# Performance work log

Hardware: AMD Instinct MI355X
Metric: run time of the kernel (lower is better)

## Reference

```python
import jax, jax.numpy as jnp
import numpy as np

B, H, S, D = 1, 16, 4096, 64


def setup_inputs() -> dict:
    key = jax.random.key(0)
    kq, kk, kv = jax.random.split(key, 3)
    Q = jax.random.normal(kq, (B, H, S, D), dtype=jnp.float32)
    K = jax.random.normal(kk, (B, H, S, D), dtype=jnp.float32)
    V = jax.random.normal(kv, (B, H, S, D), dtype=jnp.float32)
    # causal mask, broadcast over batch/heads: True = attend
    mask = jnp.tril(jnp.ones((S, S), dtype=bool))[None, None, :, :]
    return {"Q": Q, "K": K, "V": V, "mask": mask}


def reference(Q, K, V, mask):
    d_k = Q.shape[-1]
    scale = 1.0 / jnp.sqrt(jnp.asarray(d_k, dtype=Q.dtype))
    # [..., q, k] scores; mask==False positions set to -inf before softmax
    scores = jnp.einsum('...qd,...kd->...qk', Q, K) * scale
    scores = jnp.where(mask, scores, jnp.asarray(-jnp.inf, dtype=scores.dtype))
    attn = jax.nn.softmax(scores, axis=-1)
    return jnp.einsum('...qk,...kd->...qd', attn, V)
```

## Files before the change

### kernel.cpp

```cpp
#include <hip/hip_runtime.h>
#include <hip/hip_bf16.h>

typedef __attribute__((ext_vector_type(8))) short short8;
typedef __attribute__((ext_vector_type(4))) short s4v;
typedef __attribute__((ext_vector_type(4))) int   int4v;
typedef __attribute__((ext_vector_type(4))) float floatx4;

#define MFMA16(A,B,C) __builtin_amdgcn_mfma_f32_16x16x32_bf16(A,B,C,0,0,0)

__device__ __forceinline__ short bf16bits(float x) {
    __hip_bfloat16 h = __float2bfloat16(x);
    return *(short*)&h;
}
__device__ __forceinline__ short8 cvt8(const float* p) {
    floatx4 a = *(const floatx4*)p;
    floatx4 b = *(const floatx4*)(p + 4);
    short8 r;
    r[0]=bf16bits(a.x); r[1]=bf16bits(a.y); r[2]=bf16bits(a.z); r[3]=bf16bits(a.w);
    r[4]=bf16bits(b.x); r[5]=bf16bits(b.y); r[6]=bf16bits(b.z); r[7]=bf16bits(b.w);
    return r;
}
__device__ __forceinline__ short8 cvt8s(const float* p) {
    constexpr float SCL2 = 0.125f * 1.44269504088896f;
    floatx4 a = *(const floatx4*)p;
    floatx4 b = *(const floatx4*)(p + 4);
    a *= SCL2; b *= SCL2;
    short8 r;
    r[0]=bf16bits(a.x); r[1]=bf16bits(a.y); r[2]=bf16bits(a.z); r[3]=bf16bits(a.w);
    r[4]=bf16bits(b.x); r[5]=bf16bits(b.y); r[6]=bf16bits(b.z); r[7]=bf16bits(b.w);
    return r;
}
__device__ __forceinline__ int pk2(float lo, float hi) {
    int r;
    asm("v_cvt_pk_bf16_f32 %0, %1, %2" : "=v"(r) : "v"(lo), "v"(hi));
    return r;
}

__global__ __launch_bounds__(256) void prep(const float* __restrict__ V,
                                            short* __restrict__ VT,
                                            const float* __restrict__ K,
                                            short* __restrict__ K16, int doK)
{
    __shared__ short tile[64 * 65];
    const int t  = threadIdx.x;
    const int h  = blockIdx.x >> 6;
    const int s0 = (blockIdx.x & 63) << 6;
    const float* src = V + ((size_t)h * 4096 + s0) * 64;
    const int r = t >> 4, dq = (t & 15) * 4;
#pragma unroll
    for (int pass = 0; pass < 4; ++pass) {
        const int s = pass * 16 + r;
        floatx4 f = *(const floatx4*)(src + s * 64 + dq);
        short* w = tile + s * 65 + dq;
        w[0] = bf16bits(f.x); w[1] = bf16bits(f.y);
        w[2] = bf16bits(f.z); w[3] = bf16bits(f.w);
    }
    __syncthreads();
    const int d = t >> 2, sc = (t & 3) * 16;
    short8 a, b;
#pragma unroll
    for (int j = 0; j < 8; ++j) a[j] = tile[(sc + j) * 65 + d];
#pragma unroll
    for (int j = 0; j < 8; ++j) b[j] = tile[(sc + 8 + j) * 65 + d];
    short* dst = VT + ((size_t)h * 64 + d) * 4096 + s0 + sc;
    *(short8*)dst       = a;
    *(short8*)(dst + 8) = b;
    if (doK) {
        const size_t base = (size_t)blockIdx.x * 4096 + (size_t)t * 16;
        *(short8*)(K16 + base)     = cvt8(K + base);
        *(short8*)(K16 + base + 8) = cvt8(K + base + 8);
    }
}

template<bool KB16>
__global__ __attribute__((amdgpu_waves_per_eu(4, 4))) __launch_bounds__(256)
void attn_fast(const float* __restrict__ Qg, const float* __restrict__ Kg,
               const short* __restrict__ K16g, const short* __restrict__ VTg,
               float* __restrict__ Og)
{
    constexpr int S = 4096, D = 64;

    __shared__ __align__(16) short lK[8192];
    __shared__ __align__(16) short lV[8192];

    const int tid = threadIdx.x;
    const int wv  = tid >> 6;
    const int ln  = tid & 63;
    const int ll  = ln & 15;
    const int qd  = ln >> 4;
    const int qhalf = wv & 1;
    const int khalf = wv >> 1;

    const int c = blockIdx.x & 255;
    const int s = blockIdx.x >> 8;
    const int h = c & 15;
    const int x = c >> 4;
    const int qblk = (s == 0) ? (63 - x) : (s == 1) ? (32 + x) : (s == 2) ? (31 - x) : x;
    const int qb   = qblk << 6;
    const int qrow = qb + (qhalf << 5);

    const float* Qh  = Qg  + (size_t)h * S * D;
    const float* Kf  = Kg  + (size_t)h * S * D;
    const short* K16 = K16g + (size_t)h * S * D;
    const short* Vt  = VTg + (size_t)h * 64 * S;

    short8 qA0, qA1, qB0, qB1;
    {
        const float* qp = Qh + (qrow + ll) * D + qd * 8;
        qA0 = cvt8s(qp);       qA1 = cvt8s(qp + 32);
        const float* qp2 = qp + 16 * D;
        qB0 = cvt8s(qp2);      qB1 = cvt8s(qp2 + 32);
    }

    floatx4 oA[4], oB[4], olA, olB;
#pragma unroll
    for (int dt = 0; dt < 4; ++dt) { oA[dt] = (floatx4){0.f,0.f,0.f,0.f}; oB[dt] = oA[dt]; }
    olA = (floatx4){0.f,0.f,0.f,0.f};
    olB = olA;

    short8 ones;
#pragma unroll
    for (int j = 0; j < 8; ++j) ones[j] = (short)0x3F80;

    const int kkey = tid >> 3, kd8 = tid & 7;
    const int koct = kd8 & 3;
    short* kdst = lK + ((kkey >> 4) * 2 + (kd8 >> 2)) * 512
                     + ((((kkey & 15) | (koct << 4)) ^ (koct * 5)) * 8);
    const float* ksrcf = Kf  + kkey * 64 + kd8 * 8;
    const short* ksrc6 = K16 + kkey * 64 + kd8 * 8;
    const int vd = tid >> 2, voct = tid & 3;
    short* vdst = lV + (vd >> 4) * 512
                     + ((((vd & 15) | (voct << 4)) ^ (voct * 5)) * 8);
    const short* vsrc = Vt + (size_t)vd * S + voct * 8;
    const int rblk = ((ll | (qd << 4)) ^ (qd * 5));

    const int kv_end = qb + 64;
    const int wv_end = qrow + 32;

    auto ldK = [&](int kv) -> short8 {
        return KB16 ? *(const short8*)(ksrc6 + kv * 64) : cvt8(ksrcf + kv * 64);
    };

    auto mkpf = [&](floatx4 sc0, floatx4 sc1, int qgrp, int kvh) -> short8 {
        float p0[4], p1[4];
#pragma unroll
        for (int r = 0; r < 4; ++r) { p0[r] = exp2f(sc0[r]); p1[r] = exp2f(sc1[r]); }
        if (kvh + 31 > qgrp) {
            const int qg = qgrp + ll;
            const int k0 = kvh + qd * 4, k1 = k0 + 16;
#pragma unroll
            for (int r = 0; r < 4; ++r) {
                if (k0 + r > qg) p0[r] = 0.f;
                if (k1 + r > qg) p1[r] = 0.f;
            }
        }
        int w0 = pk2(p0[0], p0[1]);
        int w1 = pk2(p0[2], p0[3]);
        int w2 = pk2(p1[0], p1[1]);
        int w3 = pk2(p1[2], p1[3]);
        asm("v_permlane32_swap_b32 %0, %1" : "+v"(w0), "+v"(w2));
        asm("v_permlane32_swap_b32 %0, %1" : "+v"(w1), "+v"(w3));
        asm("v_permlane16_swap_b32 %0, %1" : "+v"(w0), "+v"(w2));
        asm("v_permlane16_swap_b32 %0, %1" : "+v"(w1), "+v"(w3));
        int4v pv = {w0, w1, w2, w3};
        return *(short8*)&pv;
    };

    short8 kp0 = ldK(0),  kp1 = ldK(32);
    short8 vp0 = *(const short8*)(vsrc);
    short8 vp1 = *(const short8*)(vsrc + 32);

    const int ntiles = kv_end >> 6;
    int bo = 0;
    for (int t = 0; t <= ntiles; ++t) {
        __syncthreads();
        if (t < ntiles) {
            *(short8*)(kdst + bo)        = kp0;
            *(short8*)(kdst + bo + 2048) = kp1;
            *(short8*)(vdst + bo)        = vp0;
            *(short8*)(vdst + bo + 2048) = vp1;
            const int nk = (t + 1) << 6;
            if (nk < kv_end) {
                kp0 = ldK(nk);
                kp1 = ldK(nk + 32);
                vp0 = *(const short8*)(vsrc + nk);
                vp1 = *(const short8*)(vsrc + nk + 32);
            }
        }
        if (t > 0) {
            const int kv  = (t - 1) << 6;
            const int kvw = kv + (khalf << 5);
            if (kvw < wv_end) {
                const int ro = (bo ^ 4096) + (khalf << 11);
                const short* Kb = lK + ro;
                const short* Vb = lV + ro;
                floatx4 zz = (floatx4){0.f,0.f,0.f,0.f};
                floatx4 sA0=zz, sA1=zz, sB0=zz, sB1=zz;
                short8 kf;
                __builtin_amdgcn_s_setprio(1);
                kf = ((const short8*)(Kb +    0))[rblk]; sA0 = MFMA16(kf, qA0, sA0); sB0 = MFMA16(kf, qB0, sB0);
                kf = ((const short8*)(Kb +  512))[rblk]; sA0 = MFMA16(kf, qA1, sA0); sB0 = MFMA16(kf, qB1, sB0);
                kf = ((const short8*)(Kb + 1024))[rblk]; sA1 = MFMA16(kf, qA0, sA1); sB1 = MFMA16(kf, qB0, sB1);
                kf = ((const short8*)(Kb + 1536))[rblk]; sA1 = MFMA16(kf, qA1, sA1); sB1 = MFMA16(kf, qB1, sB1);
                __builtin_amdgcn_s_setprio(0);

                short8 pfA = mkpf(sA0, sA1, qrow,      kvw);
                short8 pfB = mkpf(sB0, sB1, qrow + 16, kvw);
                __builtin_amdgcn_s_setprio(1);
#pragma unroll
                for (int dt = 0; dt < 4; ++dt) {
                    short8 vf = ((const short8*)(Vb + dt * 512))[rblk];
                    oA[dt] = MFMA16(pfA, vf, oA[dt]);
                    oB[dt] = MFMA16(pfB, vf, oB[dt]);
                }
                olA = MFMA16(pfA, ones, olA);
                olB = MFMA16(pfB, ones, olB);
                __builtin_amdgcn_s_setprio(0);
            }
        }
        bo ^= 4096;
    }

    __syncthreads();
    float* sAod = (float*)lK;
    float* sBod = (float*)lV;
    const int mbase = ((qhalf << 6) + ln) * 20;
    if (khalf == 1) {
#pragma unroll
        for (int dt = 0; dt < 4; ++dt)
#pragma unroll
            for (int r = 0; r < 4; ++r) {
                sAod[mbase + dt * 4 + r] = oA[dt][r];
                sBod[mbase + dt * 4 + r] = oB[dt][r];
            }
#pragma unroll
        for (int r = 0; r < 4; ++r) {
            sAod[mbase + 16 + r] = olA[r];
            sBod[mbase + 16 + r] = olB[r];
        }
    }
    __syncthreads();
    if (khalf == 0) {
#pragma unroll
        for (int dt = 0; dt < 4; ++dt)
#pragma unroll
            for (int r = 0; r < 4; ++r) {
                oA[dt][r] += sAod[mbase + dt * 4 + r];
                oB[dt][r] += sBod[mbase + dt * 4 + r];
            }
#pragma unroll
        for (int r = 0; r < 4; ++r) {
            olA[r] += sAod[mbase + 16 + r];
            olB[r] += sBod[mbase + 16 + r];
        }
#pragma unroll
        for (int r = 0; r < 4; ++r) {
            const float rl = 1.f / fmaxf(olA[r], 1e-37f);
            const int q = qrow + qd * 4 + r;
            float* op = Og + ((size_t)h * S + q) * D + ll;
#pragma unroll
            for (int dt = 0; dt < 4; ++dt)
                op[dt * 16] = oA[dt][r] * rl;
        }
#pragma unroll
        for (int r = 0; r < 4; ++r) {
            const float rl = 1.f / fmaxf(olB[r], 1e-37f);
            const int q = qrow + 16 + qd * 4 + r;
            float* op = Og + ((size_t)h * S + q) * D + ll;
#pragma unroll
            for (int dt = 0; dt < 4; ++dt)
                op[dt * 16] = oB[dt][r] * rl;
        }
    }
}

__global__ __launch_bounds__(256, 4)
void attn_legacy(const float* __restrict__ Qg, const float* __restrict__ Kg,
                 const float* __restrict__ Vg, float* __restrict__ Og)
{
    constexpr int S = 4096, D = 64;
    constexpr float SCL2 = 0.125f * 1.44269504088896f;
    constexpr float NEG  = -1.0e30f;
    __shared__ __align__(16) short lK[2048];
    __shared__ __align__(16) short lV[2048];
    __shared__ __align__(16) short lP[2048];
    const int tid = threadIdx.x, wv = tid >> 6, ln = tid & 63, ll = ln & 15, qd = ln >> 4;
    const int bid = blockIdx.x, h = bid & 15, qblk = 63 - (bid >> 4), qb = qblk << 6;
    const float* Qh = Qg + (size_t)h * S * D;
    const float* Kh = Kg + (size_t)h * S * D;
    const float* Vh = Vg + (size_t)h * S * D;
    const int qrow = qb + wv * 16;
    short8 qf0, qf1;
    { const float* qp = Qh + (qrow + ll) * D + qd * 8; qf0 = cvt8(qp); qf1 = cvt8(qp + 32); }
    floatx4 o[4]; float mi[4], li[4];
#pragma unroll
    for (int dt = 0; dt < 4; ++dt) o[dt] = (floatx4){0.f,0.f,0.f,0.f};
#pragma unroll
    for (int r = 0; r < 4; ++r) { mi[r] = NEG; li[r] = 0.f; }
    const int k_st = tid >> 3, dbase = (tid & 7) * 8;
    const int sq = (dbase >> 3) & 3, sks = dbase >> 5;
    const int kw_slot = (((k_st >> 4) * 2 + sks) * 64)
                      + (((sq << 4) | (k_st & 15)) ^ (sq | (sks << 2)));
    const int kr0 = ln ^ qd, kr1 = ln ^ (qd | 4), vbit3 = (ln >> 3) & 1;
    const int kv_end = qb + 64, wv_end = qrow + 16;
    for (int kv = 0; kv < kv_end; kv += 32) {
        __syncthreads();
        {
            short8 kval = cvt8(Kh + (kv + k_st) * D + dbase);
            ((short8*)lK)[kw_slot] = kval;
            short8 vval = cvt8(Vh + (kv + k_st) * D + dbase);
            const int vq = (k_st >> 3) << 4, vj = k_st & 7;
#pragma unroll
            for (int i = 0; i < 8; ++i) {
                int d = dbase + i, dt = d >> 4, l2 = d & 15;
                int lp = (vq | l2) ^ (((l2 >> 3) & 1) | (dt << 1));
                lV[dt * 512 + lp * 8 + vj] = vval[i];
            }
        }
        __syncthreads();
        if (kv < wv_end) {
            floatx4 sc0 = (floatx4){0.f,0.f,0.f,0.f}, sc1 = sc0; short8 kf;
            kf = ((const short8*)lK)[0*64+kr0]; sc0 = MFMA16(qf0, kf, sc0);
            kf = ((const short8*)lK)[1*64+kr1]; sc0 = MFMA16(qf1, kf, sc0);
            kf = ((const short8*)lK)[2*64+kr0]; sc1 = MFMA16(qf0, kf, sc1);
            kf = ((const short8*)lK)[3*64+kr1]; sc1 = MFMA16(qf1, kf, sc1);
            float p0[4], p1[4]; const int qg = qrow + qd * 4;
#pragma unroll
            for (int r = 0; r < 4; ++r) { p0[r] = sc0[r]*SCL2; p1[r] = sc1[r]*SCL2; }
            if (kv + 31 > qrow) {
                const int k0 = kv + ll, k1 = kv + 16 + ll;
#pragma unroll
                for (int r = 0; r < 4; ++r) {
                    if (k0 > qg + r) p0[r] = NEG;
                    if (k1 > qg + r) p1[r] = NEG;
                }
            }
#pragma unroll
            for (int r = 0; r < 4; ++r) {
                float mx = fmaxf(p0[r], p1[r]);
                mx = fmaxf(mx, __shfl_xor(mx,1)); mx = fmaxf(mx, __shfl_xor(mx,2));
                mx = fmaxf(mx, __shfl_xor(mx,4)); mx = fmaxf(mx, __shfl_xor(mx,8));
                const float nm = fmaxf(mi[r], mx);
                const float a = exp2f(mi[r] - nm); mi[r] = nm;
                p0[r] = exp2f(p0[r] - nm); p1[r] = exp2f(p1[r] - nm);
                float ps = p0[r] + p1[r];
                ps += __shfl_xor(ps,1); ps += __shfl_xor(ps,2);
                ps += __shfl_xor(ps,4); ps += __shfl_xor(ps,8);
                li[r] = li[r] * a + ps;
#pragma unroll
                for (int dt = 0; dt < 4; ++dt) o[dt][r] *= a;
            }
            {
                const int pbase = wv * 512 + (ll & 7);
                const int dl0 = ((ll >> 3) << 4) + qd * 4;
#pragma unroll
                for (int r = 0; r < 4; ++r) {
                    lP[pbase + (dl0 + r) * 8]      = bf16bits(p0[r]);
                    lP[pbase + (dl0 + 32 + r) * 8] = bf16bits(p1[r]);
                }
            }
            __threadfence_block();
            short8 pf = ((const short8*)lP)[wv * 64 + ln];
#pragma unroll
            for (int dt = 0; dt < 4; ++dt) {
                short8 vf = ((const short8*)lV)[dt * 64 + (ln ^ (vbit3 | (dt << 1)))];
                o[dt] = MFMA16(pf, vf, o[dt]);
            }
        }
    }
#pragma unroll
    for (int r = 0; r < 4; ++r) {
        const float rl = 1.f / fmaxf(li[r], 1e-30f);
        const int q = qrow + qd * 4 + r;
        float* op = Og + ((size_t)h * S + q) * D + ll;
#pragma unroll
        for (int dt = 0; dt < 4; ++dt) op[dt * 16] = o[dt][r] * rl;
    }
}

extern "C" void kernel_launch(void* const* d_in, const int* in_sizes, int n_in,
                              void* d_out, int out_size, void* d_ws, size_t ws_size,
                              hipStream_t stream) {
    const float* Q = (const float*)d_in[0];
    const float* K = (const float*)d_in[1];
    const float* V = (const float*)d_in[2];
    float* O = (float*)d_out;
    const size_t elems  = (size_t)16 * 4096 * 64;
    const size_t oneBuf = elems * sizeof(short);
    if (ws_size >= 2 * oneBuf) {
        short* VT  = (short*)d_ws;
        short* K16 = (short*)d_ws + elems;
        prep<<<dim3(1024), dim3(256), 0, stream>>>(V, VT, K, K16, 1);
        attn_fast<true><<<dim3(1024), dim3(256), 0, stream>>>(Q, K, K16, VT, O);
    } else if (ws_size >= oneBuf) {
        short* VT = (short*)d_ws;
        prep<<<dim3(1024), dim3(256), 0, stream>>>(V, VT, K, VT, 0);
        attn_fast<false><<<dim3(1024), dim3(256), 0, stream>>>(Q, K, nullptr, VT, O);
    } else {
        attn_legacy<<<dim3(1024), dim3(256), 0, stream>>>(Q, K, V, O);
    }
}
```

Measured before the change: 184.4 us.

## Split long causal query blocks across two KV halves and merge partials

Adds an attn_split kernel in which the heaviest causal query blocks (indices 33–63) are each processed by two workgroups. Each workgroup covers half of the key/value range and writes unnormalized partial outputs and row sums to workspace. A merge_split kernel then adds the partials and normalizes them. This targets the tail imbalance where the longest query blocks set the kernel time, at the cost of an extra launch, more blocks and extra global traffic for the partials. It is only used when the workspace is large enough for the partial buffers.

```diff
diff --git a/kernel.cpp b/kernel.cpp
--- a/kernel.cpp
+++ b/kernel.cpp
@@ -72,6 +72,258 @@
     }
 }
 
+__global__ __attribute__((amdgpu_waves_per_eu(4, 4))) __launch_bounds__(256)
+void attn_split(const float* __restrict__ Qg, const short* __restrict__ K16g,
+                const short* __restrict__ VTg, float* __restrict__ Og,
+                float* __restrict__ partO, float* __restrict__ partL)
+{
+    constexpr int S = 4096, D = 64;
+
+    __shared__ __align__(16) short lK[8192];
+    __shared__ __align__(16) short lV[8192];
+
+    const int tid = threadIdx.x;
+    const int wv  = tid >> 6;
+    const int ln  = tid & 63;
+    const int ll  = ln & 15;
+    const int qd  = ln >> 4;
+    const int qhalf = wv & 1;
+    const int khalf = wv >> 1;
+
+    const int bid = blockIdx.x;
+    const int h = bid / 95;
+    const int u = bid % 95;
+    int qblk, ks, ke, slot;
+    if (u < 62) {
+        qblk = 63 - (u >> 1);
+        const int part = u & 1;
+        const int T = qblk + 1, Th = T >> 1;
+        ks = part ? Th : 0;
+        ke = part ? T : Th;
+        slot = (h * 31 + (qblk - 33)) * 2 + part;
+    } else {
+        qblk = 94 - u;
+        ks = 0; ke = qblk + 1;
+        slot = -1;
+    }
+    const int qb   = qblk << 6;
+    const int qrow = qb + (qhalf << 5);
+
+    const float* Qh  = Qg  + (size_t)h * S * D;
+    const short* K16 = K16g + (size_t)h * S * D;
+    const short* Vt  = VTg + (size_t)h * 64 * S;
+
+    short8 qA0, qA1, qB0, qB1;
+    {
+        const float* qp = Qh + (qrow + ll) * D + qd * 8;
+        qA0 = cvt8s(qp);       qA1 = cvt8s(qp + 32);
+        const float* qp2 = qp + 16 * D;
+        qB0 = cvt8s(qp2);      qB1 = cvt8s(qp2 + 32);
+    }
+
+    floatx4 oA[4], oB[4], olA, olB;
+#pragma unroll
+    for (int dt = 0; dt < 4; ++dt) { oA[dt] = (floatx4){0.f,0.f,0.f,0.f}; oB[dt] = oA[dt]; }
+    olA = (floatx4){0.f,0.f,0.f,0.f};
+    olB = olA;
+
+    short8 ones;
+#pragma unroll
+    for (int j = 0; j < 8; ++j) ones[j] = (short)0x3F80;
+
+    const int kkey = tid >> 3, kd8 = tid & 7;
+    const int koct = kd8 & 3;
+    short* kdst = lK + ((kkey >> 4) * 2 + (kd8 >> 2)) * 512
+                     + ((((kkey & 15) | (koct << 4)) ^ (koct * 5)) * 8);
+    const short* ksrc6 = K16 + kkey * 64 + kd8 * 8;
+    const int vd = tid >> 2, voct = tid & 3;
+    short* vdst = lV + (vd >> 4) * 512
+                     + ((((vd & 15) | (voct << 4)) ^ (voct * 5)) * 8);
+    const short* vsrc = Vt + (size_t)vd * S + voct * 8;
+    const int rblk = ((ll | (qd << 4)) ^ (qd * 5));
+
+    const int wv_end = qrow + 32;
+
+    auto mkpf = [&](floatx4 sc0, floatx4 sc1, int qgrp, int kvh) -> short8 {
+        float p0[4], p1[4];
+#pragma unroll
+        for (int r = 0; r < 4; ++r) { p0[r] = exp2f(sc0[r]); p1[r] = exp2f(sc1[r]); }
+        if (kvh + 31 > qgrp) {
+            const int qg = qgrp + ll;
+            const int k0 = kvh + qd * 4, k1 = k0 + 16;
+#pragma unroll
+            for (int r = 0; r < 4; ++r) {
+                if (k0 + r > qg) p0[r] = 0.f;
+                if (k1 + r > qg) p1[r] = 0.f;
+            }
+        }
+        int w0 = pk2(p0[0], p0[1]);
+        int w1 = pk2(p0[2], p0[3]);
+        int w2 = pk2(p1[0], p1[1]);
+        int w3 = pk2(p1[2], p1[3]);
+        asm("v_permlane32_swap_b32 %0, %1" : "+v"(w0), "+v"(w2));
+        asm("v_permlane32_swap_b32 %0, %1" : "+v"(w1), "+v"(w3));
+        asm("v_permlane16_swap_b32 %0, %1" : "+v"(w0), "+v"(w2));
+        asm("v_permlane16_swap_b32 %0, %1" : "+v"(w1), "+v"(w3));
+        int4v pv = {w0, w1, w2, w3};
+        return *(short8*)&pv;
+    };
+
+    short8 kp0 = *(const short8*)(ksrc6 + ks * 64 * 64);
+    short8 kp1 = *(const short8*)(ksrc6 + (ks * 64 + 32) * 64);
+    short8 vp0 = *(const short8*)(vsrc + ks * 64);
+    short8 vp1 = *(const short8*)(vsrc + ks * 64 + 32);
+
+    int bo = 0;
+    for (int t = ks; t <= ke; ++t) {
+        __syncthreads();
+        if (t < ke) {
+            *(short8*)(kdst + bo)        = kp0;
+            *(short8*)(kdst + bo + 2048) = kp1;
+            *(short8*)(vdst + bo)        = vp0;
+            *(short8*)(vdst + bo + 2048) = vp1;
+            if (t + 1 < ke) {
+                const int nk = (t + 1) << 6;
+                kp0 = *(const short8*)(ksrc6 + (size_t)nk * 64);
+                kp1 = *(const short8*)(ksrc6 + (size_t)(nk + 32) * 64);
+                vp0 = *(const short8*)(vsrc + nk);
+                vp1 = *(const short8*)(vsrc + nk + 32);
+            }
+        }
+        if (t > ks) {
+            const int kv  = (t - 1) << 6;
+            const int kvw = kv + (khalf << 5);
+            if (kvw < wv_end) {
+                const int ro = (bo ^ 4096) + (khalf << 11);
+                const short* Kb = lK + ro;
+                const short* Vb = lV + ro;
+                floatx4 zz = (floatx4){0.f,0.f,0.f,0.f};
+                floatx4 sA0=zz, sA1=zz, sB0=zz, sB1=zz;
+                short8 kf;
+                __builtin_amdgcn_s_setprio(1);
+                kf = ((const short8*)(Kb +    0))[rblk]; sA0 = MFMA16(kf, qA0, sA0); sB0 = MFMA16(kf, qB0, sB0);
+                kf = ((const short8*)(Kb +  512))[rblk]; sA0 = MFMA16(kf, qA1, sA0); sB0 = MFMA16(kf, qB1, sB0);
+                kf = ((const short8*)(Kb + 1024))[rblk]; sA1 = MFMA16(kf, qA0, sA1); sB1 = MFMA16(kf, qB0, sB1);
+                kf = ((const short8*)(Kb + 1536))[rblk]; sA1 = MFMA16(kf, qA1, sA1); sB1 = MFMA16(kf, qB1, sB1);
+                __builtin_amdgcn_s_setprio(0);
+
+                short8 pfA = mkpf(sA0, sA1, qrow,      kvw);
+                short8 pfB = mkpf(sB0, sB1, qrow + 16, kvw);
+                __builtin_amdgcn_s_setprio(1);
+#pragma unroll
+                for (int dt = 0; dt < 4; ++dt) {
+                    short8 vf = ((const short8*)(Vb + dt * 512))[rblk];
+                    oA[dt] = MFMA16(pfA, vf, oA[dt]);
+                    oB[dt] = MFMA16(pfB, vf, oB[dt]);
+                }
+                olA = MFMA16(pfA, ones, olA);
+                olB = MFMA16(pfB, ones, olB);
+                __builtin_amdgcn_s_setprio(0);
+            }
+        }
+        bo ^= 4096;
+    }
+
+    __syncthreads();
+    float* sAod = (float*)lK;
+    float* sBod = (float*)lV;
+    const int mbase = ((qhalf << 6) + ln) * 20;
+    if (khalf == 1) {
+#pragma unroll
+        for (int dt = 0; dt < 4; ++dt)
+#pragma unroll
+            for (int r = 0; r < 4; ++r) {
+                sAod[mbase + dt * 4 + r] = oA[dt][r];
+                sBod[mbase + dt * 4 + r] = oB[dt][r];
+            }
+#pragma unroll
+        for (int r = 0; r < 4; ++r) {
+            sAod[mbase + 16 + r] = olA[r];
+            sBod[mbase + 16 + r] = olB[r];
+        }
+    }
+    __syncthreads();
+    if (khalf == 0) {
+#pragma unroll
+        for (int dt = 0; dt < 4; ++dt)
+#pragma unroll
+            for (int r = 0; r < 4; ++r) {
+                oA[dt][r] += sAod[mbase + dt * 4 + r];
+                oB[dt][r] += sBod[mbase + dt * 4 + r];
+            }
+#pragma unroll
+        for (int r = 0; r < 4; ++r) {
+            olA[r] += sAod[mbase + 16 + r];
+            olB[r] += sBod[mbase + 16 + r];
+        }
+        if (slot < 0) {
+#pragma unroll
+            for (int r = 0; r < 4; ++r) {
+                const float rl = 1.f / fmaxf(olA[r], 1e-37f);
+                const int q = qrow + qd * 4 + r;
+                float* op = Og + ((size_t)h * S + q) * D + ll;
+#pragma unroll
+                for (int dt = 0; dt < 4; ++dt)
+                    op[dt * 16] = oA[dt][r] * rl;
+            }
+#pragma unroll
+            for (int r = 0; r < 4; ++r) {
+                const float rl = 1.f / fmaxf(olB[r], 1e-37f);
+                const int q = qrow + 16 + qd * 4 + r;
+                float* op = Og + ((size_t)h * S + q) * D + ll;
+#pragma unroll
+                for (int dt = 0; dt < 4; ++dt)
+                    op[dt * 16] = oB[dt][r] * rl;
+            }
+        } else {
+            float* po = partO + (size_t)slot * 4096;
+            float* pl = partL + (size_t)slot * 64;
+#pragma unroll
+            for (int r = 0; r < 4; ++r) {
+                const int row = (qhalf << 5) + qd * 4 + r;
+                float* op = po + row * 64 + ll;
+#pragma unroll
+                for (int dt = 0; dt < 4; ++dt)
+                    op[dt * 16] = oA[dt][r];
+                if (ll == 0) pl[row] = olA[r];
+            }
+#pragma unroll
+            for (int r = 0; r < 4; ++r) {
+                const int row = (qhalf << 5) + 16 + qd * 4 + r;
+                float* op = po + row * 64 + ll;
+#pragma unroll
+                for (int dt = 0; dt < 4; ++dt)
+                    op[dt * 16] = oB[dt][r];
+                if (ll == 0) pl[row] = olB[r];
+            }
+        }
+    }
+}
+
+__global__ __launch_bounds__(256) void merge_split(const float* __restrict__ pO,
+                                                   const float* __restrict__ pL,
+                                                   float* __restrict__ Og)
+{
+    const int bid = blockIdx.x;
+    const int h  = bid / 31;
+    const int qb = (33 + bid % 31) << 6;
+    const size_t b0 = (size_t)(bid * 2) * 4096;
+    const int t = threadIdx.x;
+#pragma unroll
+    for (int k = 0; k < 4; ++k) {
+        const int idx = t * 4 + k * 1024;
+        const int row = idx >> 6;
+        floatx4 a = *(const floatx4*)(pO + b0 + idx);
+        floatx4 b = *(const floatx4*)(pO + b0 + 4096 + idx);
+        const float l = pL[bid * 128 + row] + pL[bid * 128 + 64 + row];
+        const float rl = 1.f / fmaxf(l, 1e-37f);
+        floatx4 o;
+        o.x = (a.x + b.x) * rl; o.y = (a.y + b.y) * rl;
+        o.z = (a.z + b.z) * rl; o.w = (a.w + b.w) * rl;
+        *(floatx4*)(Og + ((size_t)h * 4096 + qb + row) * 64 + (idx & 63)) = o;
+    }
+}
+
 template<bool KB16>
 __global__ __attribute__((amdgpu_waves_per_eu(4, 4))) __launch_bounds__(256)
 void attn_fast(const float* __restrict__ Qg, const float* __restrict__ Kg,
@@ -79,10 +331,8 @@
                float* __restrict__ Og)
 {
     constexpr int S = 4096, D = 64;
-
     __shared__ __align__(16) short lK[8192];
     __shared__ __align__(16) short lV[8192];
-
     const int tid = threadIdx.x;
     const int wv  = tid >> 6;
     const int ln  = tid & 63;
@@ -90,7 +340,6 @@
     const int qd  = ln >> 4;
     const int qhalf = wv & 1;
     const int khalf = wv >> 1;
-
     const int c = blockIdx.x & 255;
     const int s = blockIdx.x >> 8;
     const int h = c & 15;
@@ -98,12 +347,10 @@
     const int qblk = (s == 0) ? (63 - x) : (s == 1) ? (32 + x) : (s == 2) ? (31 - x) : x;
     const int qb   = qblk << 6;
     const int qrow = qb + (qhalf << 5);
-
     const float* Qh  = Qg  + (size_t)h * S * D;
     const float* Kf  = Kg  + (size_t)h * S * D;
     const short* K16 = K16g + (size_t)h * S * D;
     const short* Vt  = VTg + (size_t)h * 64 * S;
-
     short8 qA0, qA1, qB0, qB1;
     {
         const float* qp = Qh + (qrow + ll) * D + qd * 8;
@@ -111,17 +358,14 @@
         const float* qp2 = qp + 16 * D;
         qB0 = cvt8s(qp2);      qB1 = cvt8s(qp2 + 32);
     }
-
     floatx4 oA[4], oB[4], olA, olB;
 #pragma unroll
     for (int dt = 0; dt < 4; ++dt) { oA[dt] = (floatx4){0.f,0.f,0.f,0.f}; oB[dt] = oA[dt]; }
     olA = (floatx4){0.f,0.f,0.f,0.f};
     olB = olA;
-
     short8 ones;
 #pragma unroll
     for (int j = 0; j < 8; ++j) ones[j] = (short)0x3F80;
-
     const int kkey = tid >> 3, kd8 = tid & 7;
     const int koct = kd8 & 3;
     short* kdst = lK + ((kkey >> 4) * 2 + (kd8 >> 2)) * 512
@@ -133,14 +377,11 @@
                      + ((((vd & 15) | (voct << 4)) ^ (voct * 5)) * 8);
     const short* vsrc = Vt + (size_t)vd * S + voct * 8;
     const int rblk = ((ll | (qd << 4)) ^ (qd * 5));
-
     const int kv_end = qb + 64;
     const int wv_end = qrow + 32;
-
     auto ldK = [&](int kv) -> short8 {
         return KB16 ? *(const short8*)(ksrc6 + kv * 64) : cvt8(ksrcf + kv * 64);
     };
-
     auto mkpf = [&](floatx4 sc0, floatx4 sc1, int qgrp, int kvh) -> short8 {
         float p0[4], p1[4];
 #pragma unroll
@@ -165,11 +406,9 @@
         int4v pv = {w0, w1, w2, w3};
         return *(short8*)&pv;
     };
-
     short8 kp0 = ldK(0),  kp1 = ldK(32);
     short8 vp0 = *(const short8*)(vsrc);
     short8 vp1 = *(const short8*)(vsrc + 32);
-
     const int ntiles = kv_end >> 6;
     int bo = 0;
     for (int t = 0; t <= ntiles; ++t) {
@@ -203,7 +442,6 @@
                 kf = ((const short8*)(Kb + 1024))[rblk]; sA1 = MFMA16(kf, qA0, sA1); sB1 = MFMA16(kf, qB0, sB1);
                 kf = ((const short8*)(Kb + 1536))[rblk]; sA1 = MFMA16(kf, qA1, sA1); sB1 = MFMA16(kf, qB1, sB1);
                 __builtin_amdgcn_s_setprio(0);
-
                 short8 pfA = mkpf(sA0, sA1, qrow,      kvw);
                 short8 pfB = mkpf(sB0, sB1, qrow + 16, kvw);
                 __builtin_amdgcn_s_setprio(1);
@@ -220,7 +458,6 @@
         }
         bo ^= 4096;
     }
-
     __syncthreads();
     float* sAod = (float*)lK;
     float* sBod = (float*)lV;
@@ -387,7 +624,17 @@
     float* O = (float*)d_out;
     const size_t elems  = (size_t)16 * 4096 * 64;
     const size_t oneBuf = elems * sizeof(short);
-    if (ws_size >= 2 * oneBuf) {
+    const size_t partOB = (size_t)992 * 4096 * sizeof(float);
+    const size_t partLB = (size_t)992 * 64 * sizeof(float);
+    if (ws_size >= 2 * oneBuf + partOB + partLB) {
+        short* VT  = (short*)d_ws;
+        short* K16 = (short*)d_ws + elems;
+        float* pO  = (float*)((char*)d_ws + 2 * oneBuf);
+        float* pL  = pO + (size_t)992 * 4096;
+        prep<<<dim3(1024), dim3(256), 0, stream>>>(V, VT, K, K16, 1);
+        attn_split<<<dim3(1520), dim3(256), 0, stream>>>(Q, K16, VT, O, pO, pL);
+        merge_split<<<dim3(496), dim3(256), 0, stream>>>(pO, pL, O);
+    } else if (ws_size >= 2 * oneBuf) {
         short* VT  = (short*)d_ws;
         short* K16 = (short*)d_ws + elems;
         prep<<<dim3(1024), dim3(256), 0, stream>>>(V, VT, K, K16, 1);
```

New measurement: 203.5 us. 10.3% more time.
